# Kernel tuning notes

Measured on AMD Instinct MI355X. Metric: run time of the kernel, lower is better.

## Reference

```python
import jax, jax.numpy as jnp
import numpy as np
import math

B, S, E, H, D, L, HF = 8, 1024, 512, 8, 64, 6, 2048
EPS = 1e-5
INF = 1000000.0


def _gelu(x):
    # custom tanh-approx gelu from the source
    return 0.5 * x * (1 + jnp.tanh(math.sqrt(2 / math.pi) * (x + 0.044715 * x ** 3)))


def _layernorm(x, gamma, beta):
    mean = jnp.mean(x, axis=-1, keepdims=True)
    var = jnp.mean((x - mean) ** 2, axis=-1, keepdims=True)
    return gamma * ((x - mean) / jnp.sqrt(var + EPS)) + beta


def setup_inputs() -> dict:
    key = jax.random.key(0)
    ks = jax.random.split(key, 10)
    scale = 0.02
    x = jax.random.normal(ks[0], (B, S, E), dtype=jnp.float32)
    att_mask = jax.random.randint(ks[1], (B, S), 0, 2) == 1
    WQ = jax.random.normal(ks[2], (L, E, E), dtype=jnp.float32) * scale
    WK = jax.random.normal(ks[3], (L, E, E), dtype=jnp.float32) * scale
    WV = jax.random.normal(ks[4], (L, E, E), dtype=jnp.float32) * scale
    WO = jax.random.normal(ks[5], (L, E, E), dtype=jnp.float32) * scale
    W1 = jax.random.normal(ks[6], (L, HF, E), dtype=jnp.float32) * scale
    W2 = jax.random.normal(ks[7], (L, E, HF), dtype=jnp.float32) * scale
    bQ = jnp.zeros((L, E)); bK = jnp.zeros((L, E)); bV = jnp.zeros((L, E)); bO = jnp.zeros((L, E))
    b1 = jnp.zeros((L, HF)); b2 = jnp.zeros((L, E))
    g1 = jnp.ones((L, E)); bt1 = jnp.zeros((L, E))
    g2 = jnp.ones((L, E)); bt2 = jnp.zeros((L, E))
    return {"x": x, "att_mask": att_mask, "WQ": WQ, "bQ": bQ, "WK": WK, "bK": bK,
            "WV": WV, "bV": bV, "WO": WO, "bO": bO, "W1": W1, "b1": b1, "W2": W2,
            "b2": b2, "g1": g1, "bt1": bt1, "g2": g2, "bt2": bt2}


def reference(x, att_mask, WQ, bQ, WK, bK, WV, bV, WO, bO, W1, b1, W2, b2, g1, bt1, g2, bt2):
    # additive mask applied to scores: score - (~mask) * infinity, broadcast over (B,1,1,S)
    inv_att = (~att_mask).astype(x.dtype)[:, None, None, :] * INF
    inv_sqrt_d = 1.0 / math.sqrt(D)
    for l in range(L):
        # --- multi-head self-attention ---
        q = (jnp.einsum('bse,fe->bsf', x, WQ[l]) + bQ[l]).reshape(B, S, H, D).transpose(0, 2, 1, 3)
        k = (jnp.einsum('bse,fe->bsf', x, WK[l]) + bK[l]).reshape(B, S, H, D).transpose(0, 2, 1, 3)
        v = (jnp.einsum('bse,fe->bsf', x, WV[l]) + bV[l]).reshape(B, S, H, D).transpose(0, 2, 1, 3)
        score = jnp.einsum('bhsd,bhtd->bhst', q, k) * inv_sqrt_d - inv_att
        attn = jax.nn.softmax(score, axis=-1)
        o = jnp.einsum('bhst,bhtd->bhsd', attn, v).transpose(0, 2, 1, 3).reshape(B, S, E)
        o = jnp.einsum('bse,fe->bsf', o, WO[l]) + bO[l]
        x = _layernorm(x + o, g1[l], bt1[l])
        # --- pointwise feed-forward ---
        h = _gelu(jnp.einsum('bse,fe->bsf', x, W1[l]) + b1[l])
        f = jnp.einsum('bsf,ef->bse', h, W2[l]) + b2[l]
        x = _layernorm(x + f, g2[l], bt2[l])
    return x
```

## Files before the change

### kernel.cpp

```cpp
#include <hip/hip_runtime.h>
#include <cstdint>
#include <cstddef>

#define NB 8
#define NS 1024
#define NE 512
#define NH 8
#define ND 64
#define NL 6
#define NHF 2048
#define NROW (NB*NS)

typedef __bf16 bf16_t;
typedef __bf16 bf8v __attribute__((ext_vector_type(8)));
typedef __bf16 bf4v __attribute__((ext_vector_type(4)));
typedef float  f4   __attribute__((ext_vector_type(4)));

extern "C" __device__ float __ocml_native_exp2_f32(float);
#define EXP2F __ocml_native_exp2_f32
#define LOG2E 1.4426950408889634f

__device__ __forceinline__ void async_copy16(const bf16_t* g, bf16_t* l) {
    __builtin_amdgcn_global_load_lds(
        (const __attribute__((address_space(1))) void*)g,
        (__attribute__((address_space(3))) void*)l,
        16, 0, 0);
}

__device__ __forceinline__ float gelu_f(float x) {
    const float s = fmaf(0.044715f * x * x, x, x);
    const float e = EXP2F(-2.3022081995f * s);
    return x * __builtin_amdgcn_rcpf(1.0f + e);
}

template<int BN, int ACT, int OUT>
__device__ __forceinline__ void gemm_core(
    bf16_t* __restrict__ sm,
    const bf16_t* __restrict__ A, const bf16_t* __restrict__ Bm,
    const float* __restrict__ bias, bf16_t* __restrict__ Cb,
    const unsigned short* __restrict__ rank,
    int m0, int n0, int N, int K)
{
    constexpr int JN = BN / 32, WSPAN = BN / 2;
    bf16_t* As = sm;
    bf16_t* Bs = sm + 2*128*64;
    const int tid  = threadIdx.x;
    const int lane = tid & 63;
    const int wave = tid >> 6;
    const int wm = wave >> 1, wn = wave & 1;
    const int quad = lane >> 4, l16 = lane & 15;
    const int srow = tid >> 3;
    const int scol = (((tid & 7) ^ (srow & 7)) << 3);

    f4 acc[4][JN] = {};

    const bf16_t* Ag = A  + (size_t)(m0 + srow) * K + scol;
    const bf16_t* Bg = Bm + (size_t)(n0 + srow) * K + scol;
    const int sw = (l16 & 7);

    auto stage = [&](int buf, int kt) {
#pragma unroll
        for (int r = 0; r < 4; ++r)
            async_copy16(Ag + (size_t)r * 32 * K + kt, As + buf*8192 + tid*8 + r*2048);
#pragma unroll
        for (int r = 0; r < BN/32; ++r)
            async_copy16(Bg + (size_t)r * 32 * K + kt, Bs + buf*(BN*64) + tid*8 + r*2048);
    };

    stage(0, 0);
    int buf = 0;
    for (int kt = 0; kt < K; kt += 64, buf ^= 1) {
        __syncthreads();
        if (kt + 64 < K) stage(buf ^ 1, kt + 64);
        const bf16_t* Ab = As + buf*8192;
        const bf16_t* Bb = Bs + buf*(BN*64);
#pragma unroll
        for (int s = 0; s < 2; ++s) {
            const int c8 = ((s*4 + quad) ^ sw) * 8;
            bf8v af[4], bfv[JN];
#pragma unroll
            for (int i = 0; i < 4; ++i)
                af[i] = *(const bf8v*)(Ab + (wm*64 + i*16 + l16)*64 + c8);
#pragma unroll
            for (int j = 0; j < JN; ++j)
                bfv[j] = *(const bf8v*)(Bb + (wn*WSPAN + j*16 + l16)*64 + c8);
#pragma unroll
            for (int i = 0; i < 4; ++i)
#pragma unroll
                for (int j = 0; j < JN; ++j) {
                    if (OUT == 5)
                        acc[i][j] = __builtin_amdgcn_mfma_f32_16x16x32_bf16(af[i], bfv[j], acc[i][j], 0, 0, 0);
                    else
                        acc[i][j] = __builtin_amdgcn_mfma_f32_16x16x32_bf16(bfv[j], af[i], acc[i][j], 0, 0, 0);
                }
        }
    }

    if (OUT != 5) {
#pragma unroll
        for (int i = 0; i < 4; ++i) {
            const int mi = m0 + wm*64 + i*16 + l16;
            size_t m = (size_t)mi;
            if (OUT == 4) m = (size_t)((mi & ~1023) + (int)rank[mi]);
#pragma unroll
            for (int j = 0; j < JN; ++j) {
                const int nb = n0 + wn*WSPAN + j*16 + quad*4;
                const f4 bv = *(const f4*)(bias + nb);
                f4 v = acc[i][j] + bv;
                if (ACT) {
#pragma unroll
                    for (int r = 0; r < 4; ++r) v[r] = gelu_f(v[r]);
                }
                bf4v* cp = (bf4v*)(Cb + m * (size_t)N + nb);
                bf4v o;
                if (OUT == 2) {
                    const bf4v old = *cp;
#pragma unroll
                    for (int r = 0; r < 4; ++r) o[r] = (bf16_t)((float)old[r] + v[r]);
                } else {
#pragma unroll
                    for (int r = 0; r < 4; ++r) o[r] = (bf16_t)v[r];
                }
                *cp = o;
            }
        }
    } else {
#pragma unroll
        for (int j = 0; j < JN; ++j) {
            const int n = n0 + wn*WSPAN + j*16 + l16;
            const float bv = bias[n];
#pragma unroll
            for (int i = 0; i < 4; ++i) {
                const int mbase = m0 + wm*64 + i*16 + quad*4;
                const size_t b8h = (size_t)((mbase >> 10)*8 + (n >> 6));
                bf16_t* rowp = Cb + (b8h*64 + (size_t)(n & 63))*1024;
#pragma unroll
                for (int r = 0; r < 4; ++r)
                    rowp[rank[mbase + r]] = (bf16_t)(acc[i][j][r] + bv);
            }
        }
    }
}

template<int BN, int ACT, int OUT>
__global__ __launch_bounds__(256)
void gemm_bt_k(const bf16_t* __restrict__ A, const bf16_t* __restrict__ Bm,
               const float* __restrict__ bias, bf16_t* __restrict__ Cb, int N, int K)
{
    __shared__ __align__(16) bf16_t smem[2*128*64 + 2*BN*64];
    gemm_core<BN, ACT, OUT>(smem, A, Bm, bias, Cb, nullptr,
                            blockIdx.x * 128, blockIdx.y * BN, N, K);
}

__global__ __launch_bounds__(256)
void gemm_qkv_k(const bf16_t* __restrict__ A,
                const bf16_t* __restrict__ wq, const bf16_t* __restrict__ wk, const bf16_t* __restrict__ wv,
                const float* __restrict__ bq, const float* __restrict__ bk, const float* __restrict__ bv,
                bf16_t* __restrict__ Q, bf16_t* __restrict__ K, bf16_t* __restrict__ Vt,
                const unsigned short* __restrict__ rank)
{
    __shared__ __align__(16) bf16_t smem[2*128*64 + 2*128*64];
    const int mat = blockIdx.y >> 2;
    const int m0 = blockIdx.x * 128, n0 = (blockIdx.y & 3) * 128;
    if (mat == 0)      gemm_core<128, 0, 1>(smem, A, wq, bq, Q,  nullptr, m0, n0, NE, NE);
    else if (mat == 1) gemm_core<128, 0, 4>(smem, A, wk, bk, K,  rank,    m0, n0, NE, NE);
    else               gemm_core<128, 0, 5>(smem, A, wv, bv, Vt, rank,    m0, n0, NE, NE);
}

__global__ __launch_bounds__(64)
void pack_k(const int* __restrict__ m, unsigned short* __restrict__ rank,
            int* __restrict__ cntpad, float* __restrict__ maskp)
{
    const int b = blockIdx.x, lane = threadIdx.x;
    unsigned long long bals[16];
    int cnt = 0;
#pragma unroll
    for (int c = 0; c < 16; ++c) {
        const bool mk = m[b*NS + c*64 + lane] != 0;
        bals[c] = __ballot(mk);
        cnt += __popcll(bals[c]);
    }
    int u = 0, kk = 0;
#pragma unroll
    for (int c = 0; c < 16; ++c) {
        const unsigned long long bal = bals[c];
        const bool mk = (bal >> lane) & 1;
        const int pu = __popcll(bal & ((1ull << lane) - 1));
        const int r = mk ? (u + pu) : (cnt + kk + (lane - pu));
        rank[b*NS + c*64 + lane] = (unsigned short)r;
        const int cb = __popcll(bal);
        u += cb; kk += 64 - cb;
    }
    if (lane == 0) {
        int cp = (cnt + 63) & ~63;
        cntpad[b] = cp < 64 ? 64 : cp;
    }
#pragma unroll
    for (int c = 0; c < 16; ++c) {
        const int j = c*64 + lane;
        maskp[b*NS + j] = (j < cnt) ? 0.0f : -1.0e6f * LOG2E;
    }
}

__global__ __launch_bounds__(256)
void attn_k(const bf16_t* __restrict__ Q, const bf16_t* __restrict__ Kg,
            const bf16_t* __restrict__ Vt, const float* __restrict__ maskf,
            const int* __restrict__ cntpad, bf16_t* __restrict__ O)
{
    __shared__ __align__(16) bf16_t Ks[2][64*64];
    __shared__ __align__(16) bf16_t Vs[2][64*64];
    __shared__ __align__(16) bf16_t Ps[4][32*64];
    const int tid  = threadIdx.x;
    const int lane = tid & 63;
    const int wave = tid >> 6;
    const int quad = lane >> 4, l16 = lane & 15;
    const int sw = l16 & 7;
    const int bh = blockIdx.x;
    const int b = bh >> 3, h = bh & 7;
    const int q0 = blockIdx.y * 128;
    const int kend = cntpad[b];

    bf8v qf[2][2];
#pragma unroll
    for (int qi = 0; qi < 2; ++qi) {
        const bf16_t* Qp = Q + (size_t)(b*NS + q0 + wave*32 + qi*16 + l16) * NE + h*ND;
        qf[qi][0] = *(const bf8v*)(Qp + quad*8);
        qf[qi][1] = *(const bf8v*)(Qp + 32 + quad*8);
    }

    f4 oacc[2][4] = {};
    float rs[2] = {0.f, 0.f};

    const int srow = tid >> 3;
    const int scol = (((tid & 7) ^ (srow & 7)) << 3);
    const float c1 = 0.125f * LOG2E;

    auto stage = [&](int buf, int kt) {
#pragma unroll
        for (int r = 0; r < 2; ++r) {
            async_copy16(Kg + (size_t)(b*NS + kt + r*32 + srow) * NE + h*ND + scol,
                         Ks[buf] + (r*256 + tid) * 8);
            async_copy16(Vt + (size_t)(bh*ND + r*32 + srow) * NS + kt + scol,
                         Vs[buf] + (r*256 + tid) * 8);
        }
    };

    stage(0, 0);
    int buf = 0;
    for (int kt = 0; kt < kend; kt += 64, buf ^= 1) {
        __syncthreads();
        if (kt + 64 < kend) stage(buf ^ 1, kt + 64);

        f4 sacc[2][4] = {};
#pragma unroll
        for (int j = 0; j < 4; ++j) {
            bf8v kf0 = *(const bf8v*)(Ks[buf] + (j*16 + l16)*64 + ((quad    ) ^ sw)*8);
            bf8v kf1 = *(const bf8v*)(Ks[buf] + (j*16 + l16)*64 + ((quad + 4) ^ sw)*8);
#pragma unroll
            for (int qi = 0; qi < 2; ++qi) {
                sacc[qi][j] = __builtin_amdgcn_mfma_f32_16x16x32_bf16(kf0, qf[qi][0], sacc[qi][j], 0, 0, 0);
                sacc[qi][j] = __builtin_amdgcn_mfma_f32_16x16x32_bf16(kf1, qf[qi][1], sacc[qi][j], 0, 0, 0);
            }
        }

        bf16_t* Pw = Ps[wave];
#pragma unroll
        for (int j = 0; j < 4; ++j) {
            const f4 mkv = *(const f4*)(maskf + b*NS + kt + j*16 + quad*4);
#pragma unroll
            for (int qi = 0; qi < 2; ++qi) {
                bf4v o;
#pragma unroll
                for (int r = 0; r < 4; ++r) {
                    const float p = EXP2F(fmaf(sacc[qi][j][r], c1, mkv[r]));
                    rs[qi] += p;
                    o[r] = (bf16_t)p;
                }
                const int row = qi*16 + l16;
                const int chunk = (j*2 + (quad >> 1)) ^ sw;
                *(bf4v*)(Pw + row*64 + chunk*8 + (quad & 1)*4) = o;
            }
        }

#pragma unroll
        for (int ks = 0; ks < 2; ++ks) {
            bf8v pf[2];
#pragma unroll
            for (int qi = 0; qi < 2; ++qi)
                pf[qi] = *(const bf8v*)(Pw + (qi*16 + l16)*64 + ((ks*4 + quad) ^ sw)*8);
#pragma unroll
            for (int nt = 0; nt < 4; ++nt) {
                bf8v vf = *(const bf8v*)(Vs[buf] + (nt*16 + l16)*64 + ((ks*4 + quad) ^ sw)*8);
#pragma unroll
                for (int qi = 0; qi < 2; ++qi)
                    oacc[qi][nt] = __builtin_amdgcn_mfma_f32_16x16x32_bf16(vf, pf[qi], oacc[qi][nt], 0, 0, 0);
            }
        }
    }

#pragma unroll
    for (int qi = 0; qi < 2; ++qi) {
        float s = rs[qi];
        s += __shfl_xor(s, 16, 64);
        s += __shfl_xor(s, 32, 64);
        const float inv = 1.0f / s;
        const size_t row = (size_t)(b*NS + q0 + wave*32 + qi*16 + l16);
#pragma unroll
        for (int nt = 0; nt < 4; ++nt) {
            bf4v o;
#pragma unroll
            for (int r = 0; r < 4; ++r) o[r] = (bf16_t)(oacc[qi][nt][r] * inv);
            *(bf4v*)(O + row * NE + h*ND + nt*16 + quad*4) = o;
        }
    }
}

__global__ __launch_bounds__(256)
void ln_k(bf16_t* __restrict__ xb,
          const float* __restrict__ gamma, const float* __restrict__ beta,
          float* __restrict__ fout, int wf)
{
    const int row = blockIdx.x;
    const int tid = threadIdx.x;
    const size_t base = (size_t)row * NE;
    const float x0 = (float)xb[base + tid];
    const float x1 = (float)xb[base + tid + 256];
    float s  = x0 + x1;
    float ss = x0*x0 + x1*x1;
#pragma unroll
    for (int off = 32; off > 0; off >>= 1) {
        s  += __shfl_down(s,  off, 64);
        ss += __shfl_down(ss, off, 64);
    }
    __shared__ float red[8];
    const int wave = tid >> 6;
    if ((tid & 63) == 0) { red[wave] = s; red[4 + wave] = ss; }
    __syncthreads();
    s  = red[0] + red[1] + red[2] + red[3];
    ss = red[4] + red[5] + red[6] + red[7];
    const float mean = s * (1.0f / NE);
    const float var  = ss * (1.0f / NE) - mean * mean;
    const float inv  = rsqrtf(var + 1e-5f);
    const float o0 = gamma[tid]       * ((x0 - mean) * inv) + beta[tid];
    const float o1 = gamma[tid + 256] * ((x1 - mean) * inv) + beta[tid + 256];
    xb[base + tid]       = (bf16_t)o0;
    xb[base + tid + 256] = (bf16_t)o1;
    if (wf) {
        fout[base + tid]       = o0;
        fout[base + tid + 256] = o1;
    }
}

#define W4SZ ((size_t)NL*NE*NE/4)
#define WBSZ ((size_t)NL*NE*NHF/4)
#define XSZ  ((size_t)NROW*NE/4)
#define CVT_TOTAL (4*W4SZ + 2*WBSZ + XSZ)

__global__ void cvt_all(const float* __restrict__ wq, const float* __restrict__ wk,
                        const float* __restrict__ wv, const float* __restrict__ wo,
                        const float* __restrict__ w1, const float* __restrict__ w2,
                        const float* __restrict__ x,
                        bf16_t* __restrict__ owq, bf16_t* __restrict__ owk,
                        bf16_t* __restrict__ owv, bf16_t* __restrict__ owo,
                        bf16_t* __restrict__ ow1, bf16_t* __restrict__ ow2,
                        bf16_t* __restrict__ ox)
{
    size_t i = (size_t)blockIdx.x * 256 + threadIdx.x;
    if (i >= CVT_TOTAL) return;
    const float* src; bf16_t* dst;
    if      (i < 1*W4SZ)           { src = wq; dst = owq; }
    else if (i < 2*W4SZ)           { src = wk; dst = owk; i -= 1*W4SZ; }
    else if (i < 3*W4SZ)           { src = wv; dst = owv; i -= 2*W4SZ; }
    else if (i < 4*W4SZ)           { src = wo; dst = owo; i -= 3*W4SZ; }
    else if (i < 4*W4SZ + WBSZ)    { src = w1; dst = ow1; i -= 4*W4SZ; }
    else if (i < 4*W4SZ + 2*WBSZ)  { src = w2; dst = ow2; i -= 4*W4SZ + WBSZ; }
    else                           { src = x;  dst = ox;  i -= 4*W4SZ + 2*WBSZ; }
    const f4 v = ((const f4*)src)[i];
    bf4v o;
    o[0] = (bf16_t)v[0]; o[1] = (bf16_t)v[1]; o[2] = (bf16_t)v[2]; o[3] = (bf16_t)v[3];
    ((bf4v*)dst)[i] = o;
}

extern "C" void kernel_launch(void* const* d_in, const int* in_sizes, int n_in,
                              void* d_out, int out_size, void* d_ws, size_t ws_size,
                              hipStream_t stream)
{
    (void)in_sizes; (void)n_in; (void)out_size; (void)ws_size;
    const float* x   = (const float*)d_in[0];
    const int*   msk = (const int*)d_in[1];
    const float* WQ = (const float*)d_in[2];  const float* bQ  = (const float*)d_in[3];
    const float* WK = (const float*)d_in[4];  const float* bK  = (const float*)d_in[5];
    const float* WV = (const float*)d_in[6];  const float* bV  = (const float*)d_in[7];
    const float* WO = (const float*)d_in[8];  const float* bO  = (const float*)d_in[9];
    const float* W1 = (const float*)d_in[10]; const float* b1  = (const float*)d_in[11];
    const float* W2 = (const float*)d_in[12]; const float* b2  = (const float*)d_in[13];
    const float* g1 = (const float*)d_in[14]; const float* bt1 = (const float*)d_in[15];
    const float* g2 = (const float*)d_in[16]; const float* bt2 = (const float*)d_in[17];

    char* ws = (char*)d_ws;
    size_t off = 0;
    auto alloc = [&](size_t bytes) { char* p = ws + off; off += (bytes + 255) & ~(size_t)255; return p; };
    bf16_t* xb    = (bf16_t*)alloc((size_t)NROW*NE*2);
    bf16_t* Qb    = (bf16_t*)alloc((size_t)NROW*NE*2);
    bf16_t* Kb    = (bf16_t*)alloc((size_t)NROW*NE*2);
    bf16_t* Vtb   = (bf16_t*)alloc((size_t)NROW*NE*2);
    bf16_t* AOb   = (bf16_t*)alloc((size_t)NROW*NE*2);
    bf16_t* hb    = (bf16_t*)alloc((size_t)NROW*NHF*2);
    bf16_t* wqc   = (bf16_t*)alloc((size_t)NL*NE*NE*2);
    bf16_t* wkc   = (bf16_t*)alloc((size_t)NL*NE*NE*2);
    bf16_t* wvc   = (bf16_t*)alloc((size_t)NL*NE*NE*2);
    bf16_t* woc   = (bf16_t*)alloc((size_t)NL*NE*NE*2);
    bf16_t* w1c   = (bf16_t*)alloc((size_t)NL*NHF*NE*2);
    bf16_t* w2c   = (bf16_t*)alloc((size_t)NL*NE*NHF*2);
    float*  maskp = (float*) alloc((size_t)NB*NS*4);
    unsigned short* rankb = (unsigned short*)alloc((size_t)NB*NS*2);
    int*    cntp  = (int*)   alloc(NB*4);

    cvt_all<<<dim3((unsigned)((CVT_TOTAL + 255) / 256)), dim3(256), 0, stream>>>(
        WQ, WK, WV, WO, W1, W2, x, wqc, wkc, wvc, woc, w1c, w2c, xb);
    pack_k<<<dim3(NB), dim3(64), 0, stream>>>(msk, rankb, cntp, maskp);

    for (int l = 0; l < NL; ++l) {
        const bf16_t* wq  = wqc + (size_t)l*NE*NE;
        const bf16_t* wk  = wkc + (size_t)l*NE*NE;
        const bf16_t* wv  = wvc + (size_t)l*NE*NE;
        const bf16_t* wo  = woc + (size_t)l*NE*NE;
        const bf16_t* w1p = w1c + (size_t)l*NHF*NE;
        const bf16_t* w2p = w2c + (size_t)l*NE*NHF;

        gemm_qkv_k<<<dim3(64, 12), dim3(256), 0, stream>>>(
            xb, wq, wk, wv, bQ + l*NE, bK + l*NE, bV + l*NE, Qb, Kb, Vtb, rankb);
        attn_k<<<dim3(64, 8), dim3(256), 0, stream>>>(Qb, Kb, Vtb, maskp, cntp, AOb);
        gemm_bt_k<64, 0, 2><<<dim3(64, 8), dim3(256), 0, stream>>>(
            AOb, wo, bO + l*NE, xb, NE, NE);
        ln_k<<<dim3(NROW), dim3(256), 0, stream>>>(
            xb, g1 + l*NE, bt1 + l*NE, nullptr, 0);
        gemm_bt_k<128, 1, 1><<<dim3(64, 16), dim3(256), 0, stream>>>(
            xb, w1p, b1 + l*NHF, hb, NHF, NE);
        gemm_bt_k<64, 0, 2><<<dim3(64, 8), dim3(256), 0, stream>>>(
            hb, w2p, b2 + l*NE, xb, NE, NHF);
        const int last = (l == NL - 1);
        ln_k<<<dim3(NROW), dim3(256), 0, stream>>>(
            xb, g2 + l*NE, bt2 + l*NE, (float*)d_out, last);
    }
}
```

Before: 954.6 us.

## Add 256x256-tile 8-wave GEMM with staged prefetch for QKV and FFN1

Adds a new GEMM core that uses 256x256 output tiles with 512 threads (8 waves). It double-buffers A and B halves in LDS and interleaves quarter-tile MFMA phases with async global-to-LDS prefetch two K-steps ahead, using s_setprio to favour MFMA issue. The QKV projection and the first FFN GEMM switch to this kernel, and the attention kernel gets setprio around its MFMA blocks. The larger tiles cut global and LDS traffic per FLOP, but they also give fewer blocks (192 and 256 CTAs) and heavier register use, so the GPU may be under-filled.

```diff
diff --git a/kernel.cpp b/kernel.cpp
--- a/kernel.cpp
+++ b/kernel.cpp
@@ -152,19 +152,193 @@
                             blockIdx.x * 128, blockIdx.y * BN, N, K);
 }
 
-__global__ __launch_bounds__(256)
-void gemm_qkv_k(const bf16_t* __restrict__ A,
-                const bf16_t* __restrict__ wq, const bf16_t* __restrict__ wk, const bf16_t* __restrict__ wv,
-                const float* __restrict__ bq, const float* __restrict__ bk, const float* __restrict__ bv,
-                bf16_t* __restrict__ Q, bf16_t* __restrict__ K, bf16_t* __restrict__ Vt,
-                const unsigned short* __restrict__ rank)
-{
-    __shared__ __align__(16) bf16_t smem[2*128*64 + 2*128*64];
-    const int mat = blockIdx.y >> 2;
-    const int m0 = blockIdx.x * 128, n0 = (blockIdx.y & 3) * 128;
-    if (mat == 0)      gemm_core<128, 0, 1>(smem, A, wq, bq, Q,  nullptr, m0, n0, NE, NE);
-    else if (mat == 1) gemm_core<128, 0, 4>(smem, A, wk, bk, K,  rank,    m0, n0, NE, NE);
-    else               gemm_core<128, 0, 5>(smem, A, wv, bv, Vt, rank,    m0, n0, NE, NE);
+template<int ACT, int OUT>
+__device__ __forceinline__ void gemm256_core(
+    bf16_t* __restrict__ sm,
+    const bf16_t* __restrict__ A, const bf16_t* __restrict__ Bm,
+    const float* __restrict__ bias, bf16_t* __restrict__ Cb,
+    const unsigned short* __restrict__ rank,
+    int m0, int n0, int N, int K)
+{
+    const int tid  = threadIdx.x;
+    const int lane = tid & 63;
+    const int wave = tid >> 6;
+    const int wm = wave >> 2, wn = wave & 3;
+    const int quad = lane >> 4, l16 = lane & 15;
+    const int sw = l16 & 7;
+    const int srow = tid >> 3;
+    const int scol = ((tid & 7) ^ (srow & 7)) << 3;
+
+    bf16_t* As = sm;
+    bf16_t* Bs = sm + 4 * 8192;
+
+    const bf16_t* Ag = A  + (size_t)(m0 + srow) * K + scol;
+    const bf16_t* Bg = Bm + (size_t)(n0 + srow) * K + scol;
+
+    auto stageA = [&](int d, int h, int kt) {
+        bf16_t* dst = As + (d*2 + h) * 8192 + tid * 8;
+        const bf16_t* src = Ag + (size_t)(h * 128) * K + kt;
+        async_copy16(src, dst);
+        async_copy16(src + (size_t)64 * K, dst + 4096);
+    };
+    auto stageB = [&](int d, int h, int kt) {
+        bf16_t* dst = Bs + (d*2 + h) * 8192 + tid * 8;
+        const bf16_t* src = Bg + (size_t)(h * 128) * K + kt;
+        async_copy16(src, dst);
+        async_copy16(src + (size_t)64 * K, dst + 4096);
+    };
+
+    const int nt = K >> 6;
+
+    f4 acc[8][4] = {};
+    bf8v bfr[4][2], al[4][2], ah[4][2];
+
+    auto mfmaQ = [&](const bf8v (&af)[4][2], int fb, int gb) {
+#pragma unroll
+        for (int kh = 0; kh < 2; ++kh)
+#pragma unroll
+            for (int f = 0; f < 4; ++f)
+#pragma unroll
+                for (int g = 0; g < 2; ++g) {
+                    if (OUT == 5)
+                        acc[fb+f][gb+g] = __builtin_amdgcn_mfma_f32_16x16x32_bf16(af[f][kh], bfr[gb+g][kh], acc[fb+f][gb+g], 0, 0, 0);
+                    else
+                        acc[fb+f][gb+g] = __builtin_amdgcn_mfma_f32_16x16x32_bf16(bfr[gb+g][kh], af[f][kh], acc[fb+f][gb+g], 0, 0, 0);
+                }
+    };
+
+    stageB(0, 0, 0);  stageB(0, 1, 0);  stageA(0, 0, 0);  stageA(0, 1, 0);
+    stageB(1, 0, 64); stageB(1, 1, 64); stageA(1, 0, 64);
+    asm volatile("s_waitcnt vmcnt(6)" ::: "memory");
+    __builtin_amdgcn_s_barrier();
+
+    for (int t = 0; t < nt; ++t) {
+        const int d = t & 1;
+        const int kt2 = (t + 2) << 6;
+        const bf16_t* Ab = As + (d*2 + wm) * 8192;
+        const bf16_t* Bb = Bs + (d*2 + (wn >> 1)) * 8192 + (wn & 1) * 4096;
+
+#pragma unroll
+        for (int g = 0; g < 4; ++g)
+#pragma unroll
+            for (int kh = 0; kh < 2; ++kh)
+                bfr[g][kh] = *(const bf8v*)(Bb + (g*16 + l16)*64 + (((kh*4 + quad) ^ sw) << 3));
+#pragma unroll
+        for (int f = 0; f < 4; ++f)
+#pragma unroll
+            for (int kh = 0; kh < 2; ++kh)
+                al[f][kh] = *(const bf8v*)(Ab + (f*16 + l16)*64 + (((kh*4 + quad) ^ sw) << 3));
+        if (t + 1 < nt) stageA(d ^ 1, 1, (t + 1) << 6);
+        __builtin_amdgcn_s_barrier();
+        __builtin_amdgcn_s_setprio(1);
+        mfmaQ(al, 0, 0);
+        __builtin_amdgcn_s_setprio(0);
+        asm volatile("s_waitcnt lgkmcnt(0)" ::: "memory");
+        __builtin_amdgcn_s_barrier();
+
+#pragma unroll
+        for (int f = 0; f < 4; ++f)
+#pragma unroll
+            for (int kh = 0; kh < 2; ++kh)
+                ah[f][kh] = *(const bf8v*)(Ab + ((f + 4)*16 + l16)*64 + (((kh*4 + quad) ^ sw) << 3));
+        if (t + 2 < nt) stageB(d, 0, kt2);
+        __builtin_amdgcn_s_barrier();
+        __builtin_amdgcn_s_setprio(1);
+        mfmaQ(ah, 4, 0);
+        __builtin_amdgcn_s_setprio(0);
+        asm volatile("s_waitcnt lgkmcnt(0)" ::: "memory");
+        __builtin_amdgcn_s_barrier();
+
+        if (t + 2 < nt) stageB(d, 1, kt2);
+        __builtin_amdgcn_s_barrier();
+        __builtin_amdgcn_s_setprio(1);
+        mfmaQ(al, 0, 2);
+        __builtin_amdgcn_s_setprio(0);
+        asm volatile("s_waitcnt lgkmcnt(0)" ::: "memory");
+        __builtin_amdgcn_s_barrier();
+
+        if (t + 2 < nt) stageA(d, 0, kt2);
+        __builtin_amdgcn_s_barrier();
+        __builtin_amdgcn_s_setprio(1);
+        mfmaQ(ah, 4, 2);
+        __builtin_amdgcn_s_setprio(0);
+        asm volatile("s_waitcnt lgkmcnt(0)" ::: "memory");
+        if (t + 1 < nt) {
+            if (t + 2 < nt) asm volatile("s_waitcnt vmcnt(6)" ::: "memory");
+            else            asm volatile("s_waitcnt vmcnt(0)" ::: "memory");
+        }
+        __builtin_amdgcn_s_barrier();
+    }
+
+    if (OUT != 5) {
+#pragma unroll
+        for (int f = 0; f < 8; ++f) {
+            const int mi = m0 + wm*128 + f*16 + l16;
+            size_t m = (size_t)mi;
+            if (OUT == 4) m = (size_t)((mi & ~1023) + (int)rank[mi]);
+#pragma unroll
+            for (int g = 0; g < 4; ++g) {
+                const int nb = n0 + wn*64 + g*16 + quad*4;
+                const f4 bv = *(const f4*)(bias + nb);
+                f4 v = acc[f][g] + bv;
+                if (ACT) {
+#pragma unroll
+                    for (int r = 0; r < 4; ++r) v[r] = gelu_f(v[r]);
+                }
+                bf4v* cp = (bf4v*)(Cb + m * (size_t)N + nb);
+                bf4v o;
+                if (OUT == 2) {
+                    const bf4v old = *cp;
+#pragma unroll
+                    for (int r = 0; r < 4; ++r) o[r] = (bf16_t)((float)old[r] + v[r]);
+                } else {
+#pragma unroll
+                    for (int r = 0; r < 4; ++r) o[r] = (bf16_t)v[r];
+                }
+                *cp = o;
+            }
+        }
+    } else {
+#pragma unroll
+        for (int g = 0; g < 4; ++g) {
+            const int n = n0 + wn*64 + g*16 + l16;
+            const float bv = bias[n];
+#pragma unroll
+            for (int f = 0; f < 8; ++f) {
+                const int mbase = m0 + wm*128 + f*16 + quad*4;
+                const size_t b8h = (size_t)((mbase >> 10)*8 + (n >> 6));
+                bf16_t* rowp = Cb + (b8h*64 + (size_t)(n & 63))*1024;
+#pragma unroll
+                for (int r = 0; r < 4; ++r)
+                    rowp[rank[mbase + r]] = (bf16_t)(acc[f][g][r] + bv);
+            }
+        }
+    }
+}
+
+template<int ACT, int OUT>
+__global__ __launch_bounds__(512, 2)
+void gemm256_k(const bf16_t* __restrict__ A, const bf16_t* __restrict__ Bm,
+               const float* __restrict__ bias, bf16_t* __restrict__ Cb, int N, int K)
+{
+    __shared__ __align__(16) bf16_t smem[8 * 8192];
+    gemm256_core<ACT, OUT>(smem, A, Bm, bias, Cb, nullptr,
+                           blockIdx.x * 256, blockIdx.y * 256, N, K);
+}
+
+__global__ __launch_bounds__(512, 2)
+void gemm256_qkv_k(const bf16_t* __restrict__ A,
+                   const bf16_t* __restrict__ wq, const bf16_t* __restrict__ wk, const bf16_t* __restrict__ wv,
+                   const float* __restrict__ bq, const float* __restrict__ bk, const float* __restrict__ bv,
+                   bf16_t* __restrict__ Q, bf16_t* __restrict__ K, bf16_t* __restrict__ Vt,
+                   const unsigned short* __restrict__ rank)
+{
+    __shared__ __align__(16) bf16_t smem[8 * 8192];
+    const int mat = blockIdx.y >> 1;
+    const int m0 = blockIdx.x * 256, n0 = (blockIdx.y & 1) * 256;
+    if (mat == 0)      gemm256_core<0, 1>(smem, A, wq, bq, Q,  nullptr, m0, n0, NE, NE);
+    else if (mat == 1) gemm256_core<0, 4>(smem, A, wk, bk, K,  rank,    m0, n0, NE, NE);
+    else               gemm256_core<0, 5>(smem, A, wv, bv, Vt, rank,    m0, n0, NE, NE);
 }
 
 __global__ __launch_bounds__(64)
@@ -252,6 +426,7 @@
         if (kt + 64 < kend) stage(buf ^ 1, kt + 64);
 
         f4 sacc[2][4] = {};
+        __builtin_amdgcn_s_setprio(1);
 #pragma unroll
         for (int j = 0; j < 4; ++j) {
             bf8v kf0 = *(const bf8v*)(Ks[buf] + (j*16 + l16)*64 + ((quad    ) ^ sw)*8);
@@ -262,6 +437,7 @@
                 sacc[qi][j] = __builtin_amdgcn_mfma_f32_16x16x32_bf16(kf1, qf[qi][1], sacc[qi][j], 0, 0, 0);
             }
         }
+        __builtin_amdgcn_s_setprio(0);
 
         bf16_t* Pw = Ps[wave];
 #pragma unroll
@@ -282,6 +458,7 @@
             }
         }
 
+        __builtin_amdgcn_s_setprio(1);
 #pragma unroll
         for (int ks = 0; ks < 2; ++ks) {
             bf8v pf[2];
@@ -296,6 +473,7 @@
                     oacc[qi][nt] = __builtin_amdgcn_mfma_f32_16x16x32_bf16(vf, pf[qi], oacc[qi][nt], 0, 0, 0);
             }
         }
+        __builtin_amdgcn_s_setprio(0);
     }
 
 #pragma unroll
@@ -428,14 +606,14 @@
         const bf16_t* w1p = w1c + (size_t)l*NHF*NE;
         const bf16_t* w2p = w2c + (size_t)l*NE*NHF;
 
-        gemm_qkv_k<<<dim3(64, 12), dim3(256), 0, stream>>>(
+        gemm256_qkv_k<<<dim3(32, 6), dim3(512), 0, stream>>>(
             xb, wq, wk, wv, bQ + l*NE, bK + l*NE, bV + l*NE, Qb, Kb, Vtb, rankb);
         attn_k<<<dim3(64, 8), dim3(256), 0, stream>>>(Qb, Kb, Vtb, maskp, cntp, AOb);
         gemm_bt_k<64, 0, 2><<<dim3(64, 8), dim3(256), 0, stream>>>(
             AOb, wo, bO + l*NE, xb, NE, NE);
         ln_k<<<dim3(NROW), dim3(256), 0, stream>>>(
             xb, g1 + l*NE, bt1 + l*NE, nullptr, 0);
-        gemm_bt_k<128, 1, 1><<<dim3(64, 16), dim3(256), 0, stream>>>(
+        gemm256_k<1, 1><<<dim3(32, 8), dim3(512), 0, stream>>>(
             xb, w1p, b1 + l*NHF, hb, NHF, NE);
         gemm_bt_k<64, 0, 2><<<dim3(64, 8), dim3(256), 0, stream>>>(
             hb, w2p, b2 + l*NE, xb, NE, NHF);
```

Measured after the change: 1.039 ms. +8.9%, slower.
